# Kernel optimization log

Measured on AMD Instinct MI355X. Metric: run time of the kernel, lower is better.

The kernel has to match this reference:

```python
import jax, jax.numpy as jnp
import numpy as np

N, M, C, IN, OUT = 65536, 512, 512, 256, 256
EPS = 1e-8


def setup_inputs() -> dict:
    key = jax.random.key(0)
    ks = jax.random.split(key, 12)
    d = {}
    d["x"] = jax.random.normal(ks[0], (1, IN), jnp.float32)
    d["memory"] = jax.random.normal(ks[1], (1, N, M), jnp.float32) * 0.05
    d["prev_read"] = jax.random.normal(ks[2], (1, M), jnp.float32) * 0.05
    d["h"] = jnp.ones((1, C), jnp.float32)
    d["c"] = jnp.ones((1, C), jnp.float32)
    d["read_state"] = jnp.zeros((1, N), jnp.float32)
    d["write_state"] = jnp.zeros((1, N), jnp.float32)
    d["W_ih"] = jax.random.normal(ks[3], (4 * C, IN + M), jnp.float32) * 0.02
    d["b_ih"] = jax.random.normal(ks[4], (4 * C,), jnp.float32) * 0.01
    d["W_hh"] = jax.random.normal(ks[5], (4 * C, C), jnp.float32) * 0.02
    d["b_hh"] = jax.random.normal(ks[6], (4 * C,), jnp.float32) * 0.01
    d["W_read"] = jax.random.normal(ks[7], (M + 6, C), jnp.float32) * 0.02
    d["b_read"] = jnp.zeros((M + 6,), jnp.float32)
    d["W_write"] = jax.random.normal(ks[8], (3 * M + 6, C), jnp.float32) * 0.02
    d["b_write"] = jnp.zeros((3 * M + 6,), jnp.float32)
    d["W_out"] = jax.random.normal(ks[9], (OUT, C + M), jnp.float32) * 0.02
    d["b_out"] = jnp.zeros((OUT,), jnp.float32)
    return d


def _address(head_out, w_prev, memory):
    # head_out: [B, M+6(+...)]; returns sharpened addressing weights [B, N]
    key_v = head_out[:, :M]
    beta = jax.nn.softplus(head_out[:, M:M + 1])          # [B,1]
    g = jax.nn.sigmoid(head_out[:, M + 1:M + 2])          # [B,1]
    shift = jax.nn.softmax(head_out[:, M + 2:M + 5], axis=1)  # [B,3]
    gamma = 1.0 + jax.nn.softplus(head_out[:, M + 5:M + 6])   # [B,1]
    # content addressing: cosine similarity over memory rows
    a = memory + EPS                                      # [B,N,M]
    b = key_v[:, None, :] + EPS                           # [B,1,M]
    dot = jnp.sum(a * b, axis=-1)                         # [B,N]
    na = jnp.maximum(jnp.sqrt(jnp.sum(a * a, axis=-1)), EPS)
    nb = jnp.maximum(jnp.sqrt(jnp.sum(b * b, axis=-1)), EPS)
    cos = dot / (na * nb)
    w_context = jax.nn.softmax(beta * cos, axis=1)        # [B,N]
    # NOTE: original code swaps args -> g gates the PREVIOUS weights
    w_interp = g * w_prev + (1.0 - g) * w_context
    # circular shift via 3-tap correlation (conv1d with circular pad)
    w_pad = jnp.concatenate([w_interp[:, -1:], w_interp, w_interp[:, :1]], axis=1)
    w_shift = (w_pad[:, :-2] * shift[:, 0:1]
               + w_pad[:, 1:-1] * shift[:, 1:2]
               + w_pad[:, 2:] * shift[:, 2:3])
    power = w_shift ** gamma
    return power / (jnp.sum(power, axis=1, keepdims=True) + EPS)


def reference(x, memory, prev_read, h, c, read_state, write_state,
              W_ih, b_ih, W_hh, b_hh, W_read, b_read, W_write, b_write,
              W_out, b_out):
    # LSTMCell controller (torch gate order: i, f, g, o)
    inp = jnp.concatenate([x, prev_read], axis=1)                   # [B, IN+M]
    gates = inp @ W_ih.T + b_ih + h @ W_hh.T + b_hh                 # [B, 4C]
    i_g, f_g, g_g, o_g = jnp.split(gates, 4, axis=1)
    c_new = jax.nn.sigmoid(f_g) * c + jax.nn.sigmoid(i_g) * jnp.tanh(g_g)
    h_new = jax.nn.sigmoid(o_g) * jnp.tanh(c_new)

    # read head
    r_out = h_new @ W_read.T + b_read
    w_r = _address(r_out, read_state, memory)                       # [B,N]
    # faithful to torch.matmul([B,N],[B,N,M]).sum(1): sums weights over batch
    read = jnp.einsum('n,bnm->bm', jnp.sum(w_r, axis=0), memory)    # [B,M]

    # write head
    w_out_head = h_new @ W_write.T + b_write
    w_w = _address(w_out_head, write_state, memory)                 # [B,N]
    erase = jax.nn.sigmoid(w_out_head[:, M + 6:2 * M + 6])          # [B,M]
    add = w_out_head[:, 2 * M + 6:3 * M + 6]                        # [B,M]
    memory_new = memory * (1.0 - w_w[:, :, None] * erase[:, None, :]) \
                 + w_w[:, :, None] * add[:, None, :]                # [B,N,M]

    out = jax.nn.sigmoid(jnp.concatenate([h_new, read], axis=1) @ W_out.T + b_out)
    del memory_new  # state update; torch forward returns only the output
    return out
```

## Files before the change

### kernel.cpp

```cpp
#include <hip/hip_runtime.h>
#include <math.h>

#define EPS 1e-8f
#define NN 65536
#define MAGIC 1.0f

#define WS_GATES 0
#define WS_HNEW  2048
#define WS_ROUT  2560
#define WS_PMAX  3104
#define WS_PEXP  5152
#define WS_S     7200
#define WS_PSUM  72736
#define WS_PART  72992
#define WS_FLAGG 204064
#define WS_FLAGP 204192
#define WS_PART2 204448
#define WS_FLAG2 220832
#define WS_BF    262144

__device__ __forceinline__ float wave_sum(float v) {
    for (int o = 32; o > 0; o >>= 1) v += __shfl_xor(v, o);
    return v;
}
__device__ __forceinline__ float sigm(float x) { return 1.f / (1.f + expf(-x)); }
__device__ __forceinline__ float softplusf_(float x) {
    return x > 20.f ? x : log1pf(expf(x));
}
__device__ __forceinline__ float dot4(float4 a, float4 b) {
    return a.x * b.x + a.y * b.y + a.z * b.z + a.w * b.w;
}
__device__ __forceinline__ float4 ld4(const float* p) { return *(const float4*)p; }

__device__ __forceinline__ float ald(const float* p) {
    return __hip_atomic_load(p, __ATOMIC_RELAXED, __HIP_MEMORY_SCOPE_AGENT);
}
__device__ __forceinline__ float ald_acq(const float* p) {
    return __hip_atomic_load(p, __ATOMIC_ACQUIRE, __HIP_MEMORY_SCOPE_AGENT);
}
__device__ __forceinline__ void ast(float* p, float v) {
    __hip_atomic_store(p, v, __ATOMIC_RELAXED, __HIP_MEMORY_SCOPE_AGENT);
}
__device__ __forceinline__ void ast_rel(float* p, float v) {
    __hip_atomic_store(p, v, __ATOMIC_RELEASE, __HIP_MEMORY_SCOPE_AGENT);
}

__device__ __forceinline__ unsigned bf2(float a, float b) {
    unsigned ua = __float_as_uint(a), ub = __float_as_uint(b);
    unsigned ra = (ua + 0x7FFFu + ((ua >> 16) & 1u)) >> 16;
    unsigned rb = (ub + 0x7FFFu + ((ub >> 16) & 1u)) >> 16;
    return ra | (rb << 16);
}

__global__ __launch_bounds__(256) void k_front(const float* __restrict__ x,
                                               const float* __restrict__ pr,
                                               const float* __restrict__ h,
                                               const float* __restrict__ c,
                                               const float* __restrict__ W_ih,
                                               const float* __restrict__ b_ih,
                                               const float* __restrict__ W_hh,
                                               const float* __restrict__ b_hh,
                                               const float* __restrict__ W_read,
                                               const float* __restrict__ b_read,
                                               float* __restrict__ ws) {
    const int b = blockIdx.x, t = threadIdx.x;
    const int lane = t & 63, wv = t >> 6;
    __shared__ float sh[512];

    if (b < 128) {
        #pragma unroll
        for (int i = 0; i < 4; ++i) {
            const int row = b * 16 + wv * 4 + i;
            const float* wi = W_ih + (size_t)row * 768;
            const float* wh = W_hh + (size_t)row * 512;
            float acc = dot4(ld4(wi + lane * 4), ld4(x + lane * 4))
                      + dot4(ld4(wi + 256 + lane * 4), ld4(pr + lane * 4))
                      + dot4(ld4(wi + 512 + lane * 4), ld4(pr + 256 + lane * 4))
                      + dot4(ld4(wh + lane * 4), ld4(h + lane * 4))
                      + dot4(ld4(wh + 256 + lane * 4), ld4(h + 256 + lane * 4));
            acc = wave_sum(acc);
            if (lane == 0) ast(ws + WS_GATES + row, acc + b_ih[row] + b_hh[row]);
        }
        __syncthreads();
        if (t == 0) ast_rel(ws + WS_FLAGG + b, MAGIC);
    }

    if (wv == 0) {
        int cap = 0;
        for (;;) {
            float v0 = ald_acq(ws + WS_FLAGG + lane);
            float v1 = ald_acq(ws + WS_FLAGG + 64 + lane);
            if (__all(v0 == MAGIC && v1 == MAGIC)) break;
            __builtin_amdgcn_s_sleep(1);
            if (++cap > (1 << 20)) break;
        }
    }
    __syncthreads();

    for (int j = t; j < 512; j += 256) {
        float ig = ald(ws + WS_GATES + j);
        float fg = ald(ws + WS_GATES + 512 + j);
        float gg = ald(ws + WS_GATES + 1024 + j);
        float og = ald(ws + WS_GATES + 1536 + j);
        float cn = sigm(fg) * c[j] + sigm(ig) * tanhf(gg);
        float hn = sigm(og) * tanhf(cn);
        sh[j] = hn;
        if (b == 0) ws[WS_HNEW + j] = hn;
    }
    __syncthreads();
    const int o = b * 4 + wv;
    if (o < 518) {
        const float* wr = W_read + (size_t)o * 512;
        float acc = dot4(ld4(wr + lane * 4), ld4(sh + lane * 4))
                  + dot4(ld4(wr + 256 + lane * 4), ld4(sh + 256 + lane * 4));
        acc = wave_sum(acc);
        if (lane == 0) ws[WS_ROUT + o] = acc + b_read[o];
    }
}

__global__ __launch_bounds__(256) void k_cos(const float* __restrict__ mem,
                                             float* __restrict__ ws) {
    const int t = threadIdx.x, lane = t & 63, wv = t >> 6;
    const int gw = blockIdx.x * 4 + wv;
    const float* key = ws + WS_ROUT;
    unsigned short* wsb = (unsigned short*)(ws + WS_BF);
    float4 ka = ld4(key + lane * 4);
    float4 kb = ld4(key + 256 + lane * 4);
    ka.x += EPS; ka.y += EPS; ka.z += EPS; ka.w += EPS;
    kb.x += EPS; kb.y += EPS; kb.z += EPS; kb.w += EPS;
    const float nb = fmaxf(__builtin_amdgcn_sqrtf(
                        wave_sum(dot4(ka, ka) + dot4(kb, kb))), EPS);
    const float beta = softplusf_(key[512]);
    float* sp = ws + WS_S;

    float4 va[4], vb[4], xa[4], xb[4];
    #pragma unroll
    for (int i = 0; i < 4; ++i) {
        const size_t n = (size_t)gw + i * 8192;
        va[i] = ld4(mem + n * 512 + lane * 4);
        vb[i] = ld4(mem + n * 512 + 256 + lane * 4);
    }
    #pragma unroll
    for (int i = 0; i < 4; ++i) {
        const size_t n = (size_t)gw + (4 + i) * 8192;
        xa[i] = ld4(mem + n * 512 + lane * 4);
        xb[i] = ld4(mem + n * 512 + 256 + lane * 4);
    }

    float m = -1e30f, e = 0.f;
    #pragma unroll
    for (int grp = 0; grp < 2; ++grp) {
        float d[4], q[4];
        #pragma unroll
        for (int i = 0; i < 4; ++i) {
            const size_t n = (size_t)gw + (grp * 4 + i) * 8192;
            *(uint2*)(wsb + n * 512 + lane * 4) =
                make_uint2(bf2(va[i].x, va[i].y), bf2(va[i].z, va[i].w));
            *(uint2*)(wsb + n * 512 + 256 + lane * 4) =
                make_uint2(bf2(vb[i].x, vb[i].y), bf2(vb[i].z, vb[i].w));
            float4 wa = va[i], wb = vb[i];
            wa.x += EPS; wa.y += EPS; wa.z += EPS; wa.w += EPS;
            wb.x += EPS; wb.y += EPS; wb.z += EPS; wb.w += EPS;
            d[i] = dot4(wa, ka) + dot4(wb, kb);
            q[i] = dot4(wa, wa) + dot4(wb, wb);
        }
        if (grp == 0) {
            #pragma unroll
            for (int i = 0; i < 4; ++i) { va[i] = xa[i]; vb[i] = xb[i]; }
        }
        #pragma unroll
        for (int o = 32; o > 0; o >>= 1) {
            #pragma unroll
            for (int i = 0; i < 4; ++i) {
                d[i] += __shfl_xor(d[i], o);
                q[i] += __shfl_xor(q[i], o);
            }
        }
        float sv[4];
        #pragma unroll
        for (int i = 0; i < 4; ++i) {
            float na = fmaxf(__builtin_amdgcn_sqrtf(q[i]), EPS);
            sv[i] = beta * d[i] * __builtin_amdgcn_rcpf(na * nb);
        }
        float mysv = sv[0];
        if (lane == 1) mysv = sv[1];
        if (lane == 2) mysv = sv[2];
        if (lane == 3) mysv = sv[3];
        if (lane < 4) sp[gw + (grp * 4 + lane) * 8192] = mysv;
        float gm = fmaxf(fmaxf(sv[0], sv[1]), fmaxf(sv[2], sv[3]));
        float nm = fmaxf(m, gm);
        e = e * __expf(m - nm) + __expf(sv[0] - nm) + __expf(sv[1] - nm)
          + __expf(sv[2] - nm) + __expf(sv[3] - nm);
        m = nm;
    }

    __shared__ float sm[4], se[4];
    if (lane == 0) { sm[wv] = m; se[wv] = e; }
    __syncthreads();
    if (t == 0) {
        float M = fmaxf(fmaxf(sm[0], sm[1]), fmaxf(sm[2], sm[3]));
        float E = se[0] * __expf(sm[0] - M) + se[1] * __expf(sm[1] - M) +
                  se[2] * __expf(sm[2] - M) + se[3] * __expf(sm[3] - M);
        ws[WS_PMAX + blockIdx.x] = M;
        ws[WS_PEXP + blockIdx.x] = E;
    }
}

__global__ __launch_bounds__(512) void k_readout(const float* __restrict__ rs,
                                                 const float* __restrict__ W_out,
                                                 const float* __restrict__ b_out,
                                                 float* __restrict__ ws,
                                                 float* __restrict__ out) {
    const int b = blockIdx.x, t = threadIdx.x;
    const int lane = t & 63, wv = t >> 6;
    __shared__ float s_m[8], s_e[8];
    __shared__ float wi_l[258];
    __shared__ float pl[256];
    __shared__ float s_ps[4];
    __shared__ float sacc[8][512];
    __shared__ float rd[512];
    __shared__ float s_z[8];

    float m = -1e30f, e = 0.f;
    for (int i = t; i < 2048; i += 512) {
        float bm = ws[WS_PMAX + i], be = ws[WS_PEXP + i];
        float nm = fmaxf(m, bm);
        e = e * expf(m - nm) + be * expf(bm - nm);
        m = nm;
    }
    for (int o = 32; o > 0; o >>= 1) {
        float om = __shfl_xor(m, o), oe = __shfl_xor(e, o);
        float nm = fmaxf(m, om);
        e = e * expf(m - nm) + oe * expf(om - nm);
        m = nm;
    }
    if (lane == 0) { s_m[wv] = m; s_e[wv] = e; }
    __syncthreads();
    float mx = s_m[0];
    for (int i = 1; i < 8; ++i) mx = fmaxf(mx, s_m[i]);
    float Z = 0.f;
    for (int i = 0; i < 8; ++i) Z += s_e[i] * expf(s_m[i] - mx);
    const float invZ = 1.f / Z;
    const float g = sigm(ws[WS_ROUT + 513]);
    float a3 = ws[WS_ROUT + 514], b3 = ws[WS_ROUT + 515], c3 = ws[WS_ROUT + 516];
    float mm = fmaxf(a3, fmaxf(b3, c3));
    float ea = expf(a3 - mm), eb = expf(b3 - mm), ec = expf(c3 - mm);
    float ss = ea + eb + ec;
    const float s0 = ea / ss, s1 = eb / ss, s2 = ec / ss;
    const float gamma = 1.f + softplusf_(ws[WS_ROUT + 517]);

    const int start = b * 256;
    const float* sp = ws + WS_S;
    if (t < 258) {
        int idx = (start - 1 + t) & (NN - 1);
        wi_l[t] = g * rs[idx] + (1.f - g) * expf(sp[idx] - mx) * invZ;
    }
    __syncthreads();
    float ps = 0.f;
    if (t < 256) {
        float wsh = wi_l[t] * s0 + wi_l[t + 1] * s1 + wi_l[t + 2] * s2;
        float pv = powf(wsh, gamma);
        pl[t] = pv;
        ps = pv;
    }
    ps = wave_sum(ps);
    if (t < 256 && lane == 0) s_ps[wv] = ps;
    __syncthreads();
    if (t == 0) ws[WS_PSUM + b] = s_ps[0] + s_ps[1] + s_ps[2] + s_ps[3];

    {
        const unsigned short* wsb = (const unsigned short*)(ws + WS_BF);
        float a0 = 0.f, a1 = 0.f, a2 = 0.f, a3f = 0.f,
              a4 = 0.f, a5 = 0.f, a6 = 0.f, a7 = 0.f;
        #pragma unroll 4
        for (int r = wv; r < 256; r += 8) {
            float w = pl[r];
            uint4 qv = *(const uint4*)(wsb + (size_t)(start + r) * 512 + lane * 8);
            a0 += w * __uint_as_float(qv.x << 16);
            a1 += w * __uint_as_float(qv.x & 0xFFFF0000u);
            a2 += w * __uint_as_float(qv.y << 16);
            a3f += w * __uint_as_float(qv.y & 0xFFFF0000u);
            a4 += w * __uint_as_float(qv.z << 16);
            a5 += w * __uint_as_float(qv.z & 0xFFFF0000u);
            a6 += w * __uint_as_float(qv.w << 16);
            a7 += w * __uint_as_float(qv.w & 0xFFFF0000u);
        }
        float* sw = &sacc[wv][lane * 8];
        sw[0] = a0; sw[1] = a1; sw[2] = a2; sw[3] = a3f;
        sw[4] = a4; sw[5] = a5; sw[6] = a6; sw[7] = a7;
    }
    __syncthreads();
    if (t < 256) {
        const int cc = t * 2;
        float u0 = 0.f, u1 = 0.f;
        #pragma unroll
        for (int w8 = 0; w8 < 8; ++w8) {
            u0 += sacc[w8][cc];
            u1 += sacc[w8][cc + 1];
        }
        *(float2*)(ws + WS_PART + (size_t)b * 512 + cc) = make_float2(u0, u1);
    }
    __syncthreads();
    if (t == 0) ast_rel(ws + WS_FLAGP + b, MAGIC);

    if (b >= 32) return;
    if (wv == 0) {
        int cap = 0;
        for (;;) {
            float v0 = ald_acq(ws + WS_FLAGP + lane);
            float v1 = ald_acq(ws + WS_FLAGP + 64 + lane);
            float v2 = ald_acq(ws + WS_FLAGP + 128 + lane);
            float v3 = ald_acq(ws + WS_FLAGP + 192 + lane);
            if (__all(v0 == MAGIC && v1 == MAGIC && v2 == MAGIC && v3 == MAGIC))
                break;
            __builtin_amdgcn_s_sleep(1);
            if (++cap > (1 << 20)) break;
        }
    }
    __syncthreads();
    {
        float s = 0.f;
        #pragma unroll
        for (int r = 0; r < 8; ++r)
            s += ws[WS_PART + (size_t)(8 * b + r) * 512 + t];
        ws[WS_PART2 + (size_t)b * 512 + t] = s;
    }
    __syncthreads();
    if (t == 0) ast_rel(ws + WS_FLAG2 + b, MAGIC);
    if (wv == 0) {
        int cap = 0;
        for (;;) {
            float v = ald_acq(ws + WS_FLAG2 + (lane & 31));
            if (__all(v == MAGIC)) break;
            __builtin_amdgcn_s_sleep(1);
            if (++cap > (1 << 20)) break;
        }
    }
    __syncthreads();
    float z = (t < 256) ? ws[WS_PSUM + t] : 0.f;
    z = wave_sum(z);
    if (lane == 0) s_z[wv] = z;
    __syncthreads();
    float Zp = 0.f;
    for (int i = 0; i < 8; ++i) Zp += s_z[i];
    const float invZp = 1.f / (Zp + EPS);
    if (t < 256) {
        float ax = 0.f, ay = 0.f;
        #pragma unroll 8
        for (int r = 0; r < 32; ++r) {
            float2 v = *(const float2*)(ws + WS_PART2 + (size_t)r * 512 + t * 2);
            ax += v.x; ay += v.y;
        }
        rd[2 * t] = ax * invZp;
        rd[2 * t + 1] = ay * invZp;
    }
    __syncthreads();
    const int o = b * 8 + wv;
    const float* wo = W_out + (size_t)o * 1024;
    float a = dot4(ld4(wo + lane * 4), ld4(ws + WS_HNEW + lane * 4))
            + dot4(ld4(wo + 256 + lane * 4), ld4(ws + WS_HNEW + 256 + lane * 4))
            + dot4(ld4(wo + 512 + lane * 4), ld4(rd + lane * 4))
            + dot4(ld4(wo + 768 + lane * 4), ld4(rd + 256 + lane * 4));
    a = wave_sum(a);
    if (lane == 0) out[o] = sigm(a + b_out[o]);
}

extern "C" void kernel_launch(void* const* d_in, const int* in_sizes, int n_in,
                              void* d_out, int out_size, void* d_ws, size_t ws_size,
                              hipStream_t stream) {
    const float* x          = (const float*)d_in[0];
    const float* memory     = (const float*)d_in[1];
    const float* prev_read  = (const float*)d_in[2];
    const float* h          = (const float*)d_in[3];
    const float* c          = (const float*)d_in[4];
    const float* read_state = (const float*)d_in[5];
    const float* W_ih   = (const float*)d_in[7];
    const float* b_ih   = (const float*)d_in[8];
    const float* W_hh   = (const float*)d_in[9];
    const float* b_hh   = (const float*)d_in[10];
    const float* W_read = (const float*)d_in[11];
    const float* b_read = (const float*)d_in[12];
    const float* W_out  = (const float*)d_in[15];
    const float* b_out  = (const float*)d_in[16];
    float* ws  = (float*)d_ws;
    float* out = (float*)d_out;

    k_front<<<130, 256, 0, stream>>>(x, prev_read, h, c, W_ih, b_ih, W_hh, b_hh,
                                     W_read, b_read, ws);
    k_cos<<<2048, 256, 0, stream>>>(memory, ws);
    k_readout<<<256, 512, 0, stream>>>(read_state, W_out, b_out, ws, out);
}
```

Baseline: 76.01 us.

## Spread LSTM gate GEMV across 512 blocks and use fast exp/pow in readout

```diff
diff --git a/kernel.cpp b/kernel.cpp
--- a/kernel.cpp
+++ b/kernel.cpp
@@ -14,9 +14,9 @@
 #define WS_PSUM  72736
 #define WS_PART  72992
 #define WS_FLAGG 204064
-#define WS_FLAGP 204192
-#define WS_PART2 204448
-#define WS_FLAG2 220832
+#define WS_FLAGP 204576
+#define WS_FLAG2 204832
+#define WS_PART2 204864
 #define WS_BF    262144
 
 __device__ __forceinline__ float wave_sum(float v) {
@@ -67,30 +67,30 @@
     const int lane = t & 63, wv = t >> 6;
     __shared__ float sh[512];
 
-    if (b < 128) {
-        #pragma unroll
-        for (int i = 0; i < 4; ++i) {
-            const int row = b * 16 + wv * 4 + i;
-            const float* wi = W_ih + (size_t)row * 768;
-            const float* wh = W_hh + (size_t)row * 512;
-            float acc = dot4(ld4(wi + lane * 4), ld4(x + lane * 4))
-                      + dot4(ld4(wi + 256 + lane * 4), ld4(pr + lane * 4))
-                      + dot4(ld4(wi + 512 + lane * 4), ld4(pr + 256 + lane * 4))
-                      + dot4(ld4(wh + lane * 4), ld4(h + lane * 4))
-                      + dot4(ld4(wh + 256 + lane * 4), ld4(h + 256 + lane * 4));
-            acc = wave_sum(acc);
-            if (lane == 0) ast(ws + WS_GATES + row, acc + b_ih[row] + b_hh[row]);
-        }
-        __syncthreads();
-        if (t == 0) ast_rel(ws + WS_FLAGG + b, MAGIC);
-    }
+    {
+        const int row = b * 4 + wv;
+        const float* wi = W_ih + (size_t)row * 768;
+        const float* wh = W_hh + (size_t)row * 512;
+        float acc = dot4(ld4(wi + lane * 4), ld4(x + lane * 4))
+                  + dot4(ld4(wi + 256 + lane * 4), ld4(pr + lane * 4))
+                  + dot4(ld4(wi + 512 + lane * 4), ld4(pr + 256 + lane * 4))
+                  + dot4(ld4(wh + lane * 4), ld4(h + lane * 4))
+                  + dot4(ld4(wh + 256 + lane * 4), ld4(h + 256 + lane * 4));
+        acc = wave_sum(acc);
+        if (lane == 0) ast(ws + WS_GATES + row, acc + b_ih[row] + b_hh[row]);
+    }
+    __syncthreads();
+    if (t == 0) ast_rel(ws + WS_FLAGG + b, MAGIC);
+    if (b >= 130) return;
 
     if (wv == 0) {
         int cap = 0;
         for (;;) {
-            float v0 = ald_acq(ws + WS_FLAGG + lane);
-            float v1 = ald_acq(ws + WS_FLAGG + 64 + lane);
-            if (__all(v0 == MAGIC && v1 == MAGIC)) break;
+            bool ok = true;
+            #pragma unroll
+            for (int k = 0; k < 8; ++k)
+                ok &= (ald_acq(ws + WS_FLAGG + k * 64 + lane) == MAGIC);
+            if (__all(ok)) break;
             __builtin_amdgcn_s_sleep(1);
             if (++cap > (1 << 20)) break;
         }
@@ -225,13 +225,13 @@
     for (int i = t; i < 2048; i += 512) {
         float bm = ws[WS_PMAX + i], be = ws[WS_PEXP + i];
         float nm = fmaxf(m, bm);
-        e = e * expf(m - nm) + be * expf(bm - nm);
+        e = e * __expf(m - nm) + be * __expf(bm - nm);
         m = nm;
     }
     for (int o = 32; o > 0; o >>= 1) {
         float om = __shfl_xor(m, o), oe = __shfl_xor(e, o);
         float nm = fmaxf(m, om);
-        e = e * expf(m - nm) + oe * expf(om - nm);
+        e = e * __expf(m - nm) + oe * __expf(om - nm);
         m = nm;
     }
     if (lane == 0) { s_m[wv] = m; s_e[wv] = e; }
@@ -239,12 +239,12 @@
     float mx = s_m[0];
     for (int i = 1; i < 8; ++i) mx = fmaxf(mx, s_m[i]);
     float Z = 0.f;
-    for (int i = 0; i < 8; ++i) Z += s_e[i] * expf(s_m[i] - mx);
+    for (int i = 0; i < 8; ++i) Z += s_e[i] * __expf(s_m[i] - mx);
     const float invZ = 1.f / Z;
     const float g = sigm(ws[WS_ROUT + 513]);
     float a3 = ws[WS_ROUT + 514], b3 = ws[WS_ROUT + 515], c3 = ws[WS_ROUT + 516];
     float mm = fmaxf(a3, fmaxf(b3, c3));
-    float ea = expf(a3 - mm), eb = expf(b3 - mm), ec = expf(c3 - mm);
+    float ea = __expf(a3 - mm), eb = __expf(b3 - mm), ec = __expf(c3 - mm);
     float ss = ea + eb + ec;
     const float s0 = ea / ss, s1 = eb / ss, s2 = ec / ss;
     const float gamma = 1.f + softplusf_(ws[WS_ROUT + 517]);
@@ -253,13 +253,13 @@
     const float* sp = ws + WS_S;
     if (t < 258) {
         int idx = (start - 1 + t) & (NN - 1);
-        wi_l[t] = g * rs[idx] + (1.f - g) * expf(sp[idx] - mx) * invZ;
+        wi_l[t] = g * rs[idx] + (1.f - g) * __expf(sp[idx] - mx) * invZ;
     }
     __syncthreads();
     float ps = 0.f;
     if (t < 256) {
         float wsh = wi_l[t] * s0 + wi_l[t + 1] * s1 + wi_l[t + 2] * s2;
-        float pv = powf(wsh, gamma);
+        float pv = __powf(wsh, gamma);
         pl[t] = pv;
         ps = pv;
     }
@@ -269,13 +269,14 @@
     if (t == 0) ws[WS_PSUM + b] = s_ps[0] + s_ps[1] + s_ps[2] + s_ps[3];
 
     {
-        const unsigned short* wsb = (const unsigned short*)(ws + WS_BF);
+        const unsigned short* slab =
+            (const unsigned short*)(ws + WS_BF) + (size_t)(start + wv * 32) * 512;
         float a0 = 0.f, a1 = 0.f, a2 = 0.f, a3f = 0.f,
               a4 = 0.f, a5 = 0.f, a6 = 0.f, a7 = 0.f;
-        #pragma unroll 4
-        for (int r = wv; r < 256; r += 8) {
-            float w = pl[r];
-            uint4 qv = *(const uint4*)(wsb + (size_t)(start + r) * 512 + lane * 8);
+        #pragma unroll 8
+        for (int r = 0; r < 32; ++r) {
+            float w = pl[wv * 32 + r];
+            uint4 qv = *(const uint4*)(slab + (size_t)r * 512 + lane * 8);
             a0 += w * __uint_as_float(qv.x << 16);
             a1 += w * __uint_as_float(qv.x & 0xFFFF0000u);
             a2 += w * __uint_as_float(qv.y << 16);
@@ -385,7 +386,7 @@
     float* ws  = (float*)d_ws;
     float* out = (float*)d_out;
 
-    k_front<<<130, 256, 0, stream>>>(x, prev_read, h, c, W_ih, b_ih, W_hh, b_hh,
+    k_front<<<512, 256, 0, stream>>>(x, prev_read, h, c, W_ih, b_ih, W_hh, b_hh,
                                      W_read, b_read, ws);
     k_cos<<<2048, 256, 0, stream>>>(memory, ws);
     k_readout<<<256, 512, 0, stream>>>(read_state, W_out, b_out, ws, out);
```

New measurement: 83.21 us. 9.5% more time.

## Split readout into wide 2048-block read kernel and separate output reduction kernel

Applied to the files above, without the earlier changes.

```diff
diff --git a/kernel.cpp b/kernel.cpp
--- a/kernel.cpp
+++ b/kernel.cpp
@@ -11,13 +11,14 @@
 #define WS_PMAX  3104
 #define WS_PEXP  5152
 #define WS_S     7200
-#define WS_PSUM  72736
 #define WS_PART  72992
 #define WS_FLAGG 204064
 #define WS_FLAGP 204192
 #define WS_PART2 204448
 #define WS_FLAG2 220832
 #define WS_BF    262144
+#define WS_PARTB 17039360
+#define WS_PSUMB 18087936
 
 __device__ __forceinline__ float wave_sum(float v) {
     for (int o = 32; o > 0; o >>= 1) v += __shfl_xor(v, o);
@@ -206,104 +207,120 @@
     }
 }
 
-__global__ __launch_bounds__(512) void k_readout(const float* __restrict__ rs,
-                                                 const float* __restrict__ W_out,
-                                                 const float* __restrict__ b_out,
-                                                 float* __restrict__ ws,
-                                                 float* __restrict__ out) {
-    const int b = blockIdx.x, t = threadIdx.x;
+__global__ __launch_bounds__(256) void k_read(const float* __restrict__ rs,
+                                              float* __restrict__ ws) {
+    const int bb = blockIdx.x, t = threadIdx.x;
     const int lane = t & 63, wv = t >> 6;
-    __shared__ float s_m[8], s_e[8];
-    __shared__ float wi_l[258];
-    __shared__ float pl[256];
-    __shared__ float s_ps[4];
-    __shared__ float sacc[8][512];
-    __shared__ float rd[512];
-    __shared__ float s_z[8];
+    __shared__ float s_m[4], s_e[4];
+    __shared__ float wi_l[34];
+    __shared__ float pl[32];
+    __shared__ float sacc[3][512];
 
     float m = -1e30f, e = 0.f;
-    for (int i = t; i < 2048; i += 512) {
-        float bm = ws[WS_PMAX + i], be = ws[WS_PEXP + i];
+    #pragma unroll
+    for (int i = 0; i < 8; ++i) {
+        float bm = ws[WS_PMAX + t + 256 * i], be = ws[WS_PEXP + t + 256 * i];
         float nm = fmaxf(m, bm);
-        e = e * expf(m - nm) + be * expf(bm - nm);
+        e = e * __expf(m - nm) + be * __expf(bm - nm);
         m = nm;
     }
     for (int o = 32; o > 0; o >>= 1) {
         float om = __shfl_xor(m, o), oe = __shfl_xor(e, o);
         float nm = fmaxf(m, om);
-        e = e * expf(m - nm) + oe * expf(om - nm);
+        e = e * __expf(m - nm) + oe * __expf(om - nm);
         m = nm;
     }
     if (lane == 0) { s_m[wv] = m; s_e[wv] = e; }
     __syncthreads();
-    float mx = s_m[0];
-    for (int i = 1; i < 8; ++i) mx = fmaxf(mx, s_m[i]);
-    float Z = 0.f;
-    for (int i = 0; i < 8; ++i) Z += s_e[i] * expf(s_m[i] - mx);
+    const float mx = fmaxf(fmaxf(s_m[0], s_m[1]), fmaxf(s_m[2], s_m[3]));
+    const float Z = s_e[0] * __expf(s_m[0] - mx) + s_e[1] * __expf(s_m[1] - mx)
+                  + s_e[2] * __expf(s_m[2] - mx) + s_e[3] * __expf(s_m[3] - mx);
     const float invZ = 1.f / Z;
     const float g = sigm(ws[WS_ROUT + 513]);
     float a3 = ws[WS_ROUT + 514], b3 = ws[WS_ROUT + 515], c3 = ws[WS_ROUT + 516];
     float mm = fmaxf(a3, fmaxf(b3, c3));
-    float ea = expf(a3 - mm), eb = expf(b3 - mm), ec = expf(c3 - mm);
+    float ea = __expf(a3 - mm), eb = __expf(b3 - mm), ec = __expf(c3 - mm);
     float ss = ea + eb + ec;
     const float s0 = ea / ss, s1 = eb / ss, s2 = ec / ss;
     const float gamma = 1.f + softplusf_(ws[WS_ROUT + 517]);
 
-    const int start = b * 256;
-    const float* sp = ws + WS_S;
-    if (t < 258) {
+    const int start = bb * 32;
+    if (t < 34) {
         int idx = (start - 1 + t) & (NN - 1);
-        wi_l[t] = g * rs[idx] + (1.f - g) * expf(sp[idx] - mx) * invZ;
+        wi_l[t] = g * rs[idx] + (1.f - g) * __expf(ws[WS_S + idx] - mx) * invZ;
     }
     __syncthreads();
     float ps = 0.f;
-    if (t < 256) {
+    if (t < 32) {
         float wsh = wi_l[t] * s0 + wi_l[t + 1] * s1 + wi_l[t + 2] * s2;
-        float pv = powf(wsh, gamma);
+        float pv = __powf(wsh, gamma);
         pl[t] = pv;
         ps = pv;
     }
     ps = wave_sum(ps);
-    if (t < 256 && lane == 0) s_ps[wv] = ps;
-    __syncthreads();
-    if (t == 0) ws[WS_PSUM + b] = s_ps[0] + s_ps[1] + s_ps[2] + s_ps[3];
+    if (t == 0) ws[WS_PSUMB + bb] = ps;
+    __syncthreads();
+
+    const unsigned short* slab =
+        (const unsigned short*)(ws + WS_BF) + (size_t)(start + wv * 8) * 512;
+    float a0 = 0.f, a1 = 0.f, a2 = 0.f, a3f = 0.f,
+          a4 = 0.f, a5 = 0.f, a6 = 0.f, a7 = 0.f;
+    #pragma unroll
+    for (int r = 0; r < 8; ++r) {
+        float w = pl[wv * 8 + r];
+        uint4 qv = *(const uint4*)(slab + (size_t)r * 512 + lane * 8);
+        a0 += w * __uint_as_float(qv.x << 16);
+        a1 += w * __uint_as_float(qv.x & 0xFFFF0000u);
+        a2 += w * __uint_as_float(qv.y << 16);
+        a3f += w * __uint_as_float(qv.y & 0xFFFF0000u);
+        a4 += w * __uint_as_float(qv.z << 16);
+        a5 += w * __uint_as_float(qv.z & 0xFFFF0000u);
+        a6 += w * __uint_as_float(qv.w << 16);
+        a7 += w * __uint_as_float(qv.w & 0xFFFF0000u);
+    }
+    if (wv) {
+        float* sw = sacc[wv - 1];
+        sw[0 * 64 + lane] = a0; sw[1 * 64 + lane] = a1;
+        sw[2 * 64 + lane] = a2; sw[3 * 64 + lane] = a3f;
+        sw[4 * 64 + lane] = a4; sw[5 * 64 + lane] = a5;
+        sw[6 * 64 + lane] = a6; sw[7 * 64 + lane] = a7;
+    }
+    __syncthreads();
+    if (!wv) {
+        #pragma unroll
+        for (int i = 0; i < 3; ++i) {
+            const float* sw = sacc[i];
+            a0 += sw[0 * 64 + lane]; a1 += sw[1 * 64 + lane];
+            a2 += sw[2 * 64 + lane]; a3f += sw[3 * 64 + lane];
+            a4 += sw[4 * 64 + lane]; a5 += sw[5 * 64 + lane];
+            a6 += sw[6 * 64 + lane]; a7 += sw[7 * 64 + lane];
+        }
+        float* pp = ws + WS_PARTB + (size_t)bb * 512 + lane * 8;
+        *(float4*)pp = make_float4(a0, a1, a2, a3f);
+        *(float4*)(pp + 4) = make_float4(a4, a5, a6, a7);
+    }
+}
+
+__global__ __launch_bounds__(512) void k_out(const float* __restrict__ W_out,
+                                             const float* __restrict__ b_out,
+                                             float* __restrict__ ws,
+                                             float* __restrict__ out) {
+    const int b = blockIdx.x, t = threadIdx.x;
+    const int lane = t & 63, wv = t >> 6;
+    __shared__ float rd[512];
+    __shared__ float s_z[8];
 
     {
-        const unsigned short* wsb = (const unsigned short*)(ws + WS_BF);
-        float a0 = 0.f, a1 = 0.f, a2 = 0.f, a3f = 0.f,
-              a4 = 0.f, a5 = 0.f, a6 = 0.f, a7 = 0.f;
-        #pragma unroll 4
-        for (int r = wv; r < 256; r += 8) {
-            float w = pl[r];
-            uint4 qv = *(const uint4*)(wsb + (size_t)(start + r) * 512 + lane * 8);
-            a0 += w * __uint_as_float(qv.x << 16);
-            a1 += w * __uint_as_float(qv.x & 0xFFFF0000u);
-            a2 += w * __uint_as_float(qv.y << 16);
-            a3f += w * __uint_as_float(qv.y & 0xFFFF0000u);
-            a4 += w * __uint_as_float(qv.z << 16);
-            a5 += w * __uint_as_float(qv.z & 0xFFFF0000u);
-            a6 += w * __uint_as_float(qv.w << 16);
-            a7 += w * __uint_as_float(qv.w & 0xFFFF0000u);
-        }
-        float* sw = &sacc[wv][lane * 8];
-        sw[0] = a0; sw[1] = a1; sw[2] = a2; sw[3] = a3f;
-        sw[4] = a4; sw[5] = a5; sw[6] = a6; sw[7] = a7;
-    }
-    __syncthreads();
-    if (t < 256) {
-        const int cc = t * 2;
-        float u0 = 0.f, u1 = 0.f;
-        #pragma unroll
-        for (int w8 = 0; w8 < 8; ++w8) {
-            u0 += sacc[w8][cc];
-            u1 += sacc[w8][cc + 1];
-        }
-        *(float2*)(ws + WS_PART + (size_t)b * 512 + cc) = make_float2(u0, u1);
+        float s = 0.f;
+        #pragma unroll
+        for (int r = 0; r < 8; ++r)
+            s += ws[WS_PARTB + (size_t)(8 * b + r) * 512 + t];
+        ws[WS_PART + (size_t)b * 512 + t] = s;
     }
     __syncthreads();
     if (t == 0) ast_rel(ws + WS_FLAGP + b, MAGIC);
-
     if (b >= 32) return;
+
     if (wv == 0) {
         int cap = 0;
         for (;;) {
@@ -337,22 +354,21 @@
         }
     }
     __syncthreads();
-    float z = (t < 256) ? ws[WS_PSUM + t] : 0.f;
+    float z = 0.f;
+    #pragma unroll
+    for (int i = 0; i < 4; ++i) z += ws[WS_PSUMB + t + 512 * i];
     z = wave_sum(z);
     if (lane == 0) s_z[wv] = z;
     __syncthreads();
     float Zp = 0.f;
     for (int i = 0; i < 8; ++i) Zp += s_z[i];
     const float invZp = 1.f / (Zp + EPS);
-    if (t < 256) {
-        float ax = 0.f, ay = 0.f;
-        #pragma unroll 8
-        for (int r = 0; r < 32; ++r) {
-            float2 v = *(const float2*)(ws + WS_PART2 + (size_t)r * 512 + t * 2);
-            ax += v.x; ay += v.y;
-        }
-        rd[2 * t] = ax * invZp;
-        rd[2 * t + 1] = ay * invZp;
+    {
+        float s = 0.f;
+        #pragma unroll
+        for (int r = 0; r < 32; ++r)
+            s += ws[WS_PART2 + (size_t)r * 512 + t];
+        rd[t] = s * invZp;
     }
     __syncthreads();
     const int o = b * 8 + wv;
@@ -388,5 +404,6 @@
     k_front<<<130, 256, 0, stream>>>(x, prev_read, h, c, W_ih, b_ih, W_hh, b_hh,
                                      W_read, b_read, ws);
     k_cos<<<2048, 256, 0, stream>>>(memory, ws);
-    k_readout<<<256, 512, 0, stream>>>(read_state, W_out, b_out, ws, out);
-}
+    k_read<<<2048, 256, 0, stream>>>(read_state, ws);
+    k_out<<<256, 512, 0, stream>>>(W_out, b_out, ws, out);
+}
```

Measured after the change: 75.65 us. No clear change (-0.5%).
